# Kernel tuning notes

Measured on AMD Instinct MI355X. Metric: run time of the kernel, lower is better.

## Reference

```python
import jax, jax.numpy as jnp
import numpy as np

B, T, H, C = 32, 2048, 1024, 1024

def setup_inputs() -> dict:
    key = jax.random.key(0)
    k1, k2, k3, k4, k5, k6 = jax.random.split(key, 6)
    decoder_output = jax.random.normal(k1, (B, 1, H), dtype=jnp.float32)
    encoder_outputs = jax.random.normal(k2, (B, T, H), dtype=jnp.float32)
    scale = 1.0 / np.sqrt(H)
    W = jax.random.normal(k3, (H, C), dtype=jnp.float32) * scale
    V = jax.random.normal(k4, (H, C), dtype=jnp.float32) * scale
    b = jax.random.uniform(k5, (C,), dtype=jnp.float32, minval=-0.1, maxval=0.1)
    w = jax.random.normal(k6, (C, 1), dtype=jnp.float32) * (1.0 / np.sqrt(C))
    return {"decoder_output": decoder_output, "encoder_outputs": encoder_outputs,
            "W": W, "V": V, "b": b, "w": w}

def reference(decoder_output, encoder_outputs, W, V, b, w):
    # Additive (Bahdanau) content attention.
    dec_proj = jnp.einsum('bqh,hc->bqc', decoder_output, W)   # [B,1,C]
    enc_proj = jnp.einsum('bth,hc->btc', encoder_outputs, V)  # [B,T,C]
    energy = jnp.tanh(dec_proj + enc_proj + b)                # [B,T,C]
    scores = jnp.einsum('btc,c->bt', energy, w[:, 0])         # [B,T]
    alignment = jax.nn.softmax(scores, axis=-1)               # [B,T]
    context = jnp.einsum('bt,bth->bh', alignment, encoder_outputs)  # [B,H]
    return context
```

## Files before the change

### kernel.cpp

```cpp
#include <hip/hip_runtime.h>
#include <hip/hip_bf16.h>
#include <stdint.h>

#define Bn 32
#define Tn 2048
#define Hn 1024
#define Cn 1024

typedef short short8 __attribute__((ext_vector_type(8)));
typedef float floatx4 __attribute__((ext_vector_type(4)));

__device__ __forceinline__ unsigned int bf16_rne(float f) {
    union { float f; unsigned int u; } v; v.f = f;
    unsigned int u = v.u;
    return (u + 0x7fffu + ((u >> 16) & 1u)) >> 16;
}

__global__ void k_dbias(const float* __restrict__ dec, const float* __restrict__ W,
                        const float* __restrict__ bias, float* __restrict__ dbp) {
    const int b  = blockIdx.x;
    const int c  = blockIdx.y * 256 + threadIdx.x;
    const int z  = blockIdx.z;
    const int h0 = z * 256;
    const float* dv = dec + b * Hn + h0;
    const float* wp = W + (size_t)h0 * Cn + c;
    float acc = 0.f;
#pragma unroll 8
    for (int h = 0; h < 256; ++h)
        acc += dv[h] * wp[(size_t)h * Cn];
    if (z == 0) acc += bias[c];
    dbp[(size_t)(b * 4 + z) * Cn + c] = acc;
}

__global__ void k_vpack(const float* __restrict__ V, uint4* __restrict__ vp) {
    const int bid  = blockIdx.x;
    const int nt   = bid >> 5;
    const int kt   = bid & 31;
    const int lane = threadIdx.x;
    const int c    = nt * 16 + (lane & 15);
    const int k0   = kt * 32 + (lane >> 4) * 8;
    unsigned int h[8];
#pragma unroll
    for (int j = 0; j < 8; ++j)
        h[j] = bf16_rne(V[(size_t)(k0 + j) * Cn + c]);
    uint4 u;
    u.x = h[0] | (h[1] << 16);
    u.y = h[2] | (h[3] << 16);
    u.z = h[4] | (h[5] << 16);
    u.w = h[6] | (h[7] << 16);
    vp[(size_t)bid * 64 + lane] = u;
}

#define BLK_M 64
#define LDA   1032

struct ScoresShared {
    unsigned short A[BLK_M * LDA];
    float scores[BLK_M];
};

__global__ __launch_bounds__(512, 2)
void k_scores(const float* __restrict__ enc, const uint4* __restrict__ vp,
              const float* __restrict__ dbp, const float* __restrict__ wv,
              float* __restrict__ scores_g) {
    __shared__ ScoresShared sh;
    const int wg   = blockIdx.x;
    const int tid  = threadIdx.x;
    const int lane = tid & 63;
    const int wave = tid >> 6;
    const int b    = wg >> 5;
    const int row0 = wg * BLK_M;
    const int lhi  = lane >> 4;
    const int llo  = lane & 15;

    if (tid < BLK_M) sh.scores[tid] = 0.f;

    {
        const float4* ep = (const float4*)(enc + (size_t)row0 * Hn);
#pragma unroll 4
        for (int it = 0; it < 32; ++it) {
            int idx = tid + it * 512;
            int r   = idx >> 8;
            int c4  = idx & 255;
            float4 f = ep[r * 256 + c4];
            uint2 p;
            p.x = bf16_rne(f.x) | (bf16_rne(f.y) << 16);
            p.y = bf16_rne(f.z) | (bf16_rne(f.w) << 16);
            *(uint2*)&sh.A[r * LDA + c4 * 4] = p;
        }
    }
    __syncthreads();

    float score_part[16];
#pragma unroll
    for (int i = 0; i < 16; ++i) score_part[i] = 0.f;

    for (int ni = 0; ni < 2; ++ni) {
        const int colbase = (ni * 8 + wave) * 64;
        const int nt0     = colbase >> 4;

        floatx4 acc[4][4];
#pragma unroll
        for (int i = 0; i < 4; ++i)
#pragma unroll
            for (int j = 0; j < 4; ++j)
                acc[i][j] = (floatx4){0.f, 0.f, 0.f, 0.f};

#pragma unroll 2
        for (int kt = 0; kt < 32; ++kt) {
            short8 afr[4], bfr[4];
#pragma unroll
            for (int rg = 0; rg < 4; ++rg) {
                const unsigned short* ap = &sh.A[(rg * 16 + llo) * LDA + kt * 32 + lhi * 8];
                afr[rg] = *(const short8*)ap;
            }
#pragma unroll
            for (int j = 0; j < 4; ++j) {
                uint4 u = vp[((nt0 + j) * 32 + kt) * 64 + lane];
                bfr[j] = __builtin_bit_cast(short8, u);
            }
#pragma unroll
            for (int rg = 0; rg < 4; ++rg)
#pragma unroll
                for (int j = 0; j < 4; ++j)
                    acc[rg][j] = __builtin_amdgcn_mfma_f32_16x16x32_bf16(
                        afr[rg], bfr[j], acc[rg][j], 0, 0, 0);
        }

#pragma unroll
        for (int j = 0; j < 4; ++j) {
            const int c  = colbase + j * 16 + llo;
            const float db = dbp[(size_t)(b * 4 + 0) * Cn + c]
                           + dbp[(size_t)(b * 4 + 1) * Cn + c]
                           + dbp[(size_t)(b * 4 + 2) * Cn + c]
                           + dbp[(size_t)(b * 4 + 3) * Cn + c];
            const float wc = wv[c];
#pragma unroll
            for (int rg = 0; rg < 4; ++rg) {
#pragma unroll
                for (int r = 0; r < 4; ++r) {
                    float x = acc[rg][j][r] + db;
                    x = fminf(fmaxf(x, -12.f), 12.f);
                    float e = __expf(2.f * x);
                    float t = 1.f - 2.f / (e + 1.f);
                    score_part[rg * 4 + r] += t * wc;
                }
            }
        }
    }

#pragma unroll
    for (int i = 0; i < 16; ++i) {
        float v = score_part[i];
        v += __shfl_xor(v, 1);
        v += __shfl_xor(v, 2);
        v += __shfl_xor(v, 4);
        v += __shfl_xor(v, 8);
        score_part[i] = v;
    }
    if (llo == 0) {
#pragma unroll
        for (int rg = 0; rg < 4; ++rg)
#pragma unroll
            for (int r = 0; r < 4; ++r)
                atomicAdd(&sh.scores[rg * 16 + lhi * 4 + r], score_part[rg * 4 + r]);
    }
    __syncthreads();
    if (tid < BLK_M) scores_g[row0 + tid] = sh.scores[tid];
}

__global__ void k_softmax(const float* __restrict__ scores, float* __restrict__ align) {
    const int b   = blockIdx.x;
    const int tid = threadIdx.x;
    const float* s = scores + b * Tn;
    float v[8];
    float lmax = -1e30f;
#pragma unroll
    for (int i = 0; i < 8; ++i) { v[i] = s[tid + i * 256]; lmax = fmaxf(lmax, v[i]); }
    for (int off = 1; off < 64; off <<= 1) lmax = fmaxf(lmax, __shfl_xor(lmax, off));
    __shared__ float red[4];
    __shared__ float red2[4];
    if ((tid & 63) == 0) red[tid >> 6] = lmax;
    __syncthreads();
    lmax = fmaxf(fmaxf(red[0], red[1]), fmaxf(red[2], red[3]));
    float lsum = 0.f;
#pragma unroll
    for (int i = 0; i < 8; ++i) { v[i] = __expf(v[i] - lmax); lsum += v[i]; }
    for (int off = 1; off < 64; off <<= 1) lsum += __shfl_xor(lsum, off);
    if ((tid & 63) == 0) red2[tid >> 6] = lsum;
    __syncthreads();
    lsum = red2[0] + red2[1] + red2[2] + red2[3];
    const float inv = 1.f / lsum;
#pragma unroll
    for (int i = 0; i < 8; ++i) align[b * Tn + tid + i * 256] = v[i] * inv;
}

__global__ void k_ctx1(const float* __restrict__ enc, const float* __restrict__ align,
                       float* __restrict__ part) {
    const int b   = blockIdx.x;
    const int tc  = blockIdx.y;
    const int tid = threadIdx.x;
    const float4* ep = (const float4*)(enc + ((size_t)b * Tn + tc * 256) * Hn);
    const float*  al = align + b * Tn + tc * 256;
    float4 acc = {0.f, 0.f, 0.f, 0.f};
#pragma unroll 4
    for (int t = 0; t < 256; ++t) {
        const float a = al[t];
        const float4 e = ep[t * 256 + tid];
        acc.x += a * e.x; acc.y += a * e.y; acc.z += a * e.z; acc.w += a * e.w;
    }
    ((float4*)part)[(b * 8 + tc) * 256 + tid] = acc;
}

__global__ void k_ctx2(const float* __restrict__ part, float* __restrict__ out) {
    const int b   = blockIdx.x;
    const int tid = threadIdx.x;
    const float4* pp = (const float4*)part;
    float4 s = {0.f, 0.f, 0.f, 0.f};
#pragma unroll
    for (int tc = 0; tc < 8; ++tc) {
        float4 p = pp[(b * 8 + tc) * 256 + tid];
        s.x += p.x; s.y += p.y; s.z += p.z; s.w += p.w;
    }
    ((float4*)out)[b * 256 + tid] = s;
}

extern "C" void kernel_launch(void* const* d_in, const int* in_sizes, int n_in,
                              void* d_out, int out_size, void* d_ws, size_t ws_size,
                              hipStream_t stream) {
    const float* dec  = (const float*)d_in[0];
    const float* enc  = (const float*)d_in[1];
    const float* W    = (const float*)d_in[2];
    const float* V    = (const float*)d_in[3];
    const float* bias = (const float*)d_in[4];
    const float* wv   = (const float*)d_in[5];
    float* out = (float*)d_out;

    char* ws = (char*)d_ws;
    float* dbp    = (float*)(ws);
    uint4* vpack  = (uint4*)(ws + 524288);
    float* scores = (float*)(ws + 524288 + 2097152);
    float* align  = (float*)(ws + 524288 + 2097152 + 262144);
    float* cpart  = (float*)(ws + 524288 + 2097152 + 262144 + 262144);

    k_dbias  <<<dim3(32, 4, 4), 256, 0, stream>>>(dec, W, bias, dbp);
    k_vpack  <<<2048, 64, 0, stream>>>(V, vpack);
    k_scores <<<1024, 512, 0, stream>>>(enc, vpack, dbp, wv, scores);
    k_softmax<<<32, 256, 0, stream>>>(scores, align);
    k_ctx1   <<<dim3(32, 8), 256, 0, stream>>>(enc, align, cpart);
    k_ctx2   <<<32, 256, 0, stream>>>(cpart, out);
}
```

Measured before the change: 570.4 us.

## Persistent scores kernel with register prefetch; merge prep and softmax kernels

```diff
diff --git a/kernel.cpp b/kernel.cpp
--- a/kernel.cpp
+++ b/kernel.cpp
@@ -16,39 +16,44 @@
     return (u + 0x7fffu + ((u >> 16) & 1u)) >> 16;
 }
 
-__global__ void k_dbias(const float* __restrict__ dec, const float* __restrict__ W,
-                        const float* __restrict__ bias, float* __restrict__ dbp) {
-    const int b  = blockIdx.x;
-    const int c  = blockIdx.y * 256 + threadIdx.x;
-    const int z  = blockIdx.z;
-    const int h0 = z * 256;
-    const float* dv = dec + b * Hn + h0;
-    const float* wp = W + (size_t)h0 * Cn + c;
-    float acc = 0.f;
+__global__ void k_prep(const float* __restrict__ dec, const float* __restrict__ W,
+                       const float* __restrict__ bias, const float* __restrict__ V,
+                       float* __restrict__ dbp, uint4* __restrict__ vp) {
+    if (blockIdx.x < 512) {
+        const int blk = blockIdx.x;
+        const int b  = blk >> 4;
+        const int y  = (blk >> 2) & 3;
+        const int z  = blk & 3;
+        const int c  = y * 256 + threadIdx.x;
+        const int h0 = z * 256;
+        const float* dv = dec + b * Hn + h0;
+        const float* wp = W + (size_t)h0 * Cn + c;
+        float acc = 0.f;
 #pragma unroll 8
-    for (int h = 0; h < 256; ++h)
-        acc += dv[h] * wp[(size_t)h * Cn];
-    if (z == 0) acc += bias[c];
-    dbp[(size_t)(b * 4 + z) * Cn + c] = acc;
-}
-
-__global__ void k_vpack(const float* __restrict__ V, uint4* __restrict__ vp) {
-    const int bid  = blockIdx.x;
-    const int nt   = bid >> 5;
-    const int kt   = bid & 31;
-    const int lane = threadIdx.x;
-    const int c    = nt * 16 + (lane & 15);
-    const int k0   = kt * 32 + (lane >> 4) * 8;
-    unsigned int h[8];
-#pragma unroll
-    for (int j = 0; j < 8; ++j)
-        h[j] = bf16_rne(V[(size_t)(k0 + j) * Cn + c]);
-    uint4 u;
-    u.x = h[0] | (h[1] << 16);
-    u.y = h[2] | (h[3] << 16);
-    u.z = h[4] | (h[5] << 16);
-    u.w = h[6] | (h[7] << 16);
-    vp[(size_t)bid * 64 + lane] = u;
+        for (int h = 0; h < 256; ++h)
+            acc += dv[h] * wp[(size_t)h * Cn];
+        if (z == 0) acc += bias[c];
+        dbp[(size_t)(b * 4 + z) * Cn + c] = acc;
+    } else {
+        const int vb   = blockIdx.x - 512;
+        const int sub  = threadIdx.x >> 6;
+        const int lane = threadIdx.x & 63;
+        const int bid  = vb * 4 + sub;
+        const int nt   = bid >> 5;
+        const int kt   = bid & 31;
+        const int c    = nt * 16 + (lane & 15);
+        const int k0   = kt * 32 + (lane >> 4) * 8;
+        unsigned int h[8];
+#pragma unroll
+        for (int j = 0; j < 8; ++j)
+            h[j] = bf16_rne(V[(size_t)(k0 + j) * Cn + c]);
+        uint4 u;
+        u.x = h[0] | (h[1] << 16);
+        u.y = h[2] | (h[3] << 16);
+        u.z = h[4] | (h[5] << 16);
+        u.w = h[6] | (h[7] << 16);
+        vp[(size_t)bid * 64 + lane] = u;
+    }
 }
 
 #define BLK_M 64
@@ -64,148 +69,159 @@
               const float* __restrict__ dbp, const float* __restrict__ wv,
               float* __restrict__ scores_g) {
     __shared__ ScoresShared sh;
-    const int wg   = blockIdx.x;
     const int tid  = threadIdx.x;
     const int lane = tid & 63;
     const int wave = tid >> 6;
-    const int b    = wg >> 5;
-    const int row0 = wg * BLK_M;
     const int lhi  = lane >> 4;
     const int llo  = lane & 15;
 
-    if (tid < BLK_M) sh.scores[tid] = 0.f;
-
+    float4 fbuf[32];
     {
-        const float4* ep = (const float4*)(enc + (size_t)row0 * Hn);
-#pragma unroll 4
-        for (int it = 0; it < 32; ++it) {
-            int idx = tid + it * 512;
+        const float4* ep = (const float4*)(enc + (size_t)(blockIdx.x * 4) * BLK_M * Hn);
+#pragma unroll
+        for (int i = 0; i < 32; ++i)
+            fbuf[i] = ep[tid + i * 512];
+    }
+
+    for (int q = 0; q < 4; ++q) {
+        const int tile = blockIdx.x * 4 + q;
+        const int b    = tile >> 5;
+        const int row0 = tile * BLK_M;
+
+        if (tid < BLK_M) sh.scores[tid] = 0.f;
+
+#pragma unroll
+        for (int i = 0; i < 32; ++i) {
+            int idx = tid + i * 512;
             int r   = idx >> 8;
             int c4  = idx & 255;
-            float4 f = ep[r * 256 + c4];
             uint2 p;
-            p.x = bf16_rne(f.x) | (bf16_rne(f.y) << 16);
-            p.y = bf16_rne(f.z) | (bf16_rne(f.w) << 16);
+            p.x = bf16_rne(fbuf[i].x) | (bf16_rne(fbuf[i].y) << 16);
+            p.y = bf16_rne(fbuf[i].z) | (bf16_rne(fbuf[i].w) << 16);
             *(uint2*)&sh.A[r * LDA + c4 * 4] = p;
         }
-    }
-    __syncthreads();
-
-    float score_part[16];
-#pragma unroll
-    for (int i = 0; i < 16; ++i) score_part[i] = 0.f;
-
-    for (int ni = 0; ni < 2; ++ni) {
-        const int colbase = (ni * 8 + wave) * 64;
-        const int nt0     = colbase >> 4;
-
-        floatx4 acc[4][4];
-#pragma unroll
-        for (int i = 0; i < 4; ++i)
-#pragma unroll
-            for (int j = 0; j < 4; ++j)
-                acc[i][j] = (floatx4){0.f, 0.f, 0.f, 0.f};
+        __syncthreads();
+
+        if (q < 3) {
+            const float4* ep = (const float4*)(enc + (size_t)(tile + 1) * BLK_M * Hn);
+#pragma unroll
+            for (int i = 0; i < 32; ++i)
+                fbuf[i] = ep[tid + i * 512];
+        }
+
+        float score_part[16];
+#pragma unroll
+        for (int i = 0; i < 16; ++i) score_part[i] = 0.f;
+
+        for (int ni = 0; ni < 2; ++ni) {
+            const int colbase = (ni * 8 + wave) * 64;
+            const int nt0     = colbase >> 4;
+
+            floatx4 acc[4][4];
+#pragma unroll
+            for (int i = 0; i < 4; ++i)
+#pragma unroll
+                for (int j = 0; j < 4; ++j)
+                    acc[i][j] = (floatx4){0.f, 0.f, 0.f, 0.f};
 
 #pragma unroll 2
-        for (int kt = 0; kt < 32; ++kt) {
-            short8 afr[4], bfr[4];
-#pragma unroll
-            for (int rg = 0; rg < 4; ++rg) {
-                const unsigned short* ap = &sh.A[(rg * 16 + llo) * LDA + kt * 32 + lhi * 8];
-                afr[rg] = *(const short8*)ap;
+            for (int kt = 0; kt < 32; ++kt) {
+                short8 afr[4], bfr[4];
+#pragma unroll
+                for (int rg = 0; rg < 4; ++rg) {
+                    const unsigned short* ap = &sh.A[(rg * 16 + llo) * LDA + kt * 32 + lhi * 8];
+                    afr[rg] = *(const short8*)ap;
+                }
+#pragma unroll
+                for (int j = 0; j < 4; ++j) {
+                    uint4 u = vp[((nt0 + j) * 32 + kt) * 64 + lane];
+                    bfr[j] = __builtin_bit_cast(short8, u);
+                }
+#pragma unroll
+                for (int rg = 0; rg < 4; ++rg)
+#pragma unroll
+                    for (int j = 0; j < 4; ++j)
+                        acc[rg][j] = __builtin_amdgcn_mfma_f32_16x16x32_bf16(
+                            afr[rg], bfr[j], acc[rg][j], 0, 0, 0);
             }
+
 #pragma unroll
             for (int j = 0; j < 4; ++j) {
-                uint4 u = vp[((nt0 + j) * 32 + kt) * 64 + lane];
-                bfr[j] = __builtin_bit_cast(short8, u);
-            }
-#pragma unroll
-            for (int rg = 0; rg < 4; ++rg)
-#pragma unroll
-                for (int j = 0; j < 4; ++j)
-                    acc[rg][j] = __builtin_amdgcn_mfma_f32_16x16x32_bf16(
-                        afr[rg], bfr[j], acc[rg][j], 0, 0, 0);
-        }
-
-#pragma unroll
-        for (int j = 0; j < 4; ++j) {
-            const int c  = colbase + j * 16 + llo;
-            const float db = dbp[(size_t)(b * 4 + 0) * Cn + c]
-                           + dbp[(size_t)(b * 4 + 1) * Cn + c]
-                           + dbp[(size_t)(b * 4 + 2) * Cn + c]
-                           + dbp[(size_t)(b * 4 + 3) * Cn + c];
-            const float wc = wv[c];
-#pragma unroll
-            for (int rg = 0; rg < 4; ++rg) {
-#pragma unroll
-                for (int r = 0; r < 4; ++r) {
-                    float x = acc[rg][j][r] + db;
-                    x = fminf(fmaxf(x, -12.f), 12.f);
-                    float e = __expf(2.f * x);
-                    float t = 1.f - 2.f / (e + 1.f);
-                    score_part[rg * 4 + r] += t * wc;
+                const int c  = colbase + j * 16 + llo;
+                const float db = dbp[(size_t)(b * 4 + 0) * Cn + c]
+                               + dbp[(size_t)(b * 4 + 1) * Cn + c]
+                               + dbp[(size_t)(b * 4 + 2) * Cn + c]
+                               + dbp[(size_t)(b * 4 + 3) * Cn + c];
+                const float wc = wv[c];
+#pragma unroll
+                for (int rg = 0; rg < 4; ++rg) {
+#pragma unroll
+                    for (int r = 0; r < 4; ++r) {
+                        float x = acc[rg][j][r] + db;
+                        x = fminf(fmaxf(x, -12.f), 12.f);
+                        float e = __expf(2.f * x);
+                        float t = 1.f - 2.f / (e + 1.f);
+                        score_part[rg * 4 + r] += t * wc;
+                    }
                 }
             }
         }
-    }
-
-#pragma unroll
-    for (int i = 0; i < 16; ++i) {
-        float v = score_part[i];
-        v += __shfl_xor(v, 1);
-        v += __shfl_xor(v, 2);
-        v += __shfl_xor(v, 4);
-        v += __shfl_xor(v, 8);
-        score_part[i] = v;
-    }
-    if (llo == 0) {
-#pragma unroll
-        for (int rg = 0; rg < 4; ++rg)
-#pragma unroll
-            for (int r = 0; r < 4; ++r)
-                atomicAdd(&sh.scores[rg * 16 + lhi * 4 + r], score_part[rg * 4 + r]);
-    }
-    __syncthreads();
-    if (tid < BLK_M) scores_g[row0 + tid] = sh.scores[tid];
-}
-
-__global__ void k_softmax(const float* __restrict__ scores, float* __restrict__ align) {
+
+#pragma unroll
+        for (int i = 0; i < 16; ++i) {
+            float v = score_part[i];
+            v += __shfl_xor(v, 1);
+            v += __shfl_xor(v, 2);
+            v += __shfl_xor(v, 4);
+            v += __shfl_xor(v, 8);
+            score_part[i] = v;
+        }
+        if (llo == 0) {
+#pragma unroll
+            for (int rg = 0; rg < 4; ++rg)
+#pragma unroll
+                for (int r = 0; r < 4; ++r)
+                    atomicAdd(&sh.scores[rg * 16 + lhi * 4 + r], score_part[rg * 4 + r]);
+        }
+        __syncthreads();
+        if (tid < BLK_M) scores_g[row0 + tid] = sh.scores[tid];
+    }
+}
+
+__global__ void k_ctx1(const float* __restrict__ enc, const float* __restrict__ scores,
+                       float* __restrict__ part) {
     const int b   = blockIdx.x;
+    const int tc  = blockIdx.y;
     const int tid = threadIdx.x;
+    __shared__ float al_sh[256];
+    __shared__ float red[4];
+    __shared__ float red2[4];
+
     const float* s = scores + b * Tn;
     float v[8];
     float lmax = -1e30f;
 #pragma unroll
     for (int i = 0; i < 8; ++i) { v[i] = s[tid + i * 256]; lmax = fmaxf(lmax, v[i]); }
     for (int off = 1; off < 64; off <<= 1) lmax = fmaxf(lmax, __shfl_xor(lmax, off));
-    __shared__ float red[4];
-    __shared__ float red2[4];
     if ((tid & 63) == 0) red[tid >> 6] = lmax;
     __syncthreads();
     lmax = fmaxf(fmaxf(red[0], red[1]), fmaxf(red[2], red[3]));
     float lsum = 0.f;
 #pragma unroll
-    for (int i = 0; i < 8; ++i) { v[i] = __expf(v[i] - lmax); lsum += v[i]; }
+    for (int i = 0; i < 8; ++i) lsum += __expf(v[i] - lmax);
     for (int off = 1; off < 64; off <<= 1) lsum += __shfl_xor(lsum, off);
     if ((tid & 63) == 0) red2[tid >> 6] = lsum;
     __syncthreads();
     lsum = red2[0] + red2[1] + red2[2] + red2[3];
     const float inv = 1.f / lsum;
-#pragma unroll
-    for (int i = 0; i < 8; ++i) align[b * Tn + tid + i * 256] = v[i] * inv;
-}
-
-__global__ void k_ctx1(const float* __restrict__ enc, const float* __restrict__ align,
-                       float* __restrict__ part) {
-    const int b   = blockIdx.x;
-    const int tc  = blockIdx.y;
-    const int tid = threadIdx.x;
+    al_sh[tid] = __expf(s[tc * 256 + tid] - lmax) * inv;
+    __syncthreads();
+
     const float4* ep = (const float4*)(enc + ((size_t)b * Tn + tc * 256) * Hn);
-    const float*  al = align + b * Tn + tc * 256;
     float4 acc = {0.f, 0.f, 0.f, 0.f};
 #pragma unroll 4
     for (int t = 0; t < 256; ++t) {
-        const float a = al[t];
+        const float a = al_sh[t];
         const float4 e = ep[t * 256 + tid];
         acc.x += a * e.x; acc.y += a * e.y; acc.z += a * e.z; acc.w += a * e.w;
     }
@@ -240,13 +256,10 @@
     float* dbp    = (float*)(ws);
     uint4* vpack  = (uint4*)(ws + 524288);
     float* scores = (float*)(ws + 524288 + 2097152);
-    float* align  = (float*)(ws + 524288 + 2097152 + 262144);
-    float* cpart  = (float*)(ws + 524288 + 2097152 + 262144 + 262144);
-
-    k_dbias  <<<dim3(32, 4, 4), 256, 0, stream>>>(dec, W, bias, dbp);
-    k_vpack  <<<2048, 64, 0, stream>>>(V, vpack);
-    k_scores <<<1024, 512, 0, stream>>>(enc, vpack, dbp, wv, scores);
-    k_softmax<<<32, 256, 0, stream>>>(scores, align);
-    k_ctx1   <<<dim3(32, 8), 256, 0, stream>>>(enc, align, cpart);
-    k_ctx2   <<<32, 256, 0, stream>>>(cpart, out);
-}
+    float* cpart  = (float*)(ws + 524288 + 2097152 + 262144);
+
+    k_prep  <<<1024, 256, 0, stream>>>(dec, W, bias, V, dbp, vpack);
+    k_scores<<<256, 512, 0, stream>>>(enc, vpack, dbp, wv, scores);
+    k_ctx1  <<<dim3(32, 8), 256, 0, stream>>>(enc, scores, cpart);
+    k_ctx2  <<<32, 256, 0, stream>>>(cpart, out);
+}
```

After: 649.3 us. 13.8% more time.
